# Kernel tuning notes

Hardware: AMD Instinct MI355X
Metric: run time of the kernel (lower is better)

## Reference

```python
import jax, jax.numpy as jnp
import numpy as np
from jax import lax

WIN = 15      # sliding window size
BINS = 64     # luminance histogram bins
ALPHA = 0.9   # local vs global histogram mix
LAM1 = 0.5    # a-channel (material) removal weight
LAM2 = 0.5    # b-channel (material) removal weight
EPS = 1e-6


def _box_sum(x, win):
    return lax.reduce_window(x, 0.0, lax.add, (1, win, win, 1), (1, 1, 1, 1), 'SAME')


def setup_inputs() -> dict:
    key = jax.random.key(0)
    u = jax.random.uniform(key, (4, 3, 512, 512), dtype=jnp.float32)
    L = u[:, 0] * 100.0                 # L in [0,100]
    a = u[:, 1] * 255.0 - 128.0         # a in [-128,127]
    b = u[:, 2] * 255.0 - 128.0         # b in [-128,127]
    return {"batch_lab_raw": jnp.stack([L, a, b], axis=1)}


def reference(batch_lab_raw):
    # Normalize channels
    Ln = jnp.clip(batch_lab_raw[:, 0] / 100.0, 0.0, 1.0)      # (B,H,W)
    an = (batch_lab_raw[:, 1] + 128.0) / 255.0                # (B,H,W)
    bn = (batch_lab_raw[:, 2] + 128.0) / 255.0                # (B,H,W)

    # --- windowed luminance histogram anomaly ---
    idx = jnp.clip((Ln * BINS).astype(jnp.int32), 0, BINS - 1)            # (B,H,W)
    onehot = jax.nn.one_hot(idx, BINS, dtype=Ln.dtype)                    # (B,H,W,K)
    cnt = _box_sum(onehot, WIN)                                           # (B,H,W,K)
    n = _box_sum(jnp.ones(Ln.shape + (1,), Ln.dtype), WIN)                # (B,H,W,1) valid-pixel count
    # probability of own bin within local window
    p_loc = jnp.take_along_axis(cnt / n, idx[..., None], axis=-1)[..., 0]  # (B,H,W)
    # global per-image histogram probability of own bin
    p_glob_bins = jnp.mean(onehot, axis=(1, 2))                            # (B,K)
    p_glob = jnp.einsum('bhwk,bk->bhw', onehot, p_glob_bins)              # (B,H,W)

    S = -jnp.log(ALPHA * p_loc + (1.0 - ALPHA) * p_glob + EPS)            # surprise
    S_min = jnp.min(S, axis=(1, 2), keepdims=True)
    S_max = jnp.max(S, axis=(1, 2), keepdims=True)
    L_anom_norm = (S - S_min) / (S_max - S_min + EPS)                     # (B,H,W)

    # --- de-materialized illumination: remove local chroma (material) variation ---
    mu_a = _box_sum(an[..., None], WIN)[..., 0] / n[..., 0]
    mu_b = _box_sum(bn[..., None], WIN)[..., 0] / n[..., 0]
    L_perp = jnp.clip(Ln - LAM1 * (an - mu_a) - LAM2 * (bn - mu_b), 0.0, 1.0)

    return (L_perp[:, None], L_anom_norm[:, None])  # each (B,1,H,W)
```

## Files before the change

kernel.cpp:

```cpp
#include <hip/hip_runtime.h>

#define Hh 512
#define Ww 512
#define NPIX (Hh*Ww)
#define BATCH 4


__global__ __launch_bounds__(256) void k_hist(const float* __restrict__ in,
                                              unsigned* __restrict__ hp) {
    __shared__ unsigned lh[64];
    const int tid = threadIdx.x;
    if (tid < 64) lh[tid] = 0u;
    __syncthreads();
    const int img = blockIdx.x >> 6, sub = blockIdx.x & 63;
    const float4* Lp = (const float4*)(in + (size_t)img * 3 * NPIX) + sub * 1024;
    #pragma unroll
    for (int t = 0; t < 4; ++t) {
        float4 v = Lp[t*256 + tid];
        float f[4] = {v.x, v.y, v.z, v.w};
        #pragma unroll
        for (int j = 0; j < 4; ++j) {
            float ln = fminf(fmaxf(f[j] / 100.0f, 0.0f), 1.0f);
            int idx = min((int)(ln * 64.0f), 63);
            atomicAdd(&lh[idx], 1u);
        }
    }
    __syncthreads();
    if (tid < 64) hp[((size_t)img*64 + tid)*64 + sub] = lh[tid];
}

__global__ __launch_bounds__(256, 4) void k_main(const float* __restrict__ in,
        const unsigned* __restrict__ hp, float* __restrict__ bmin,
        float* __restrict__ bmax, float* __restrict__ out)
{
    __shared__ unsigned s_pk[78*9];
    __shared__ float s_c[78*36];
    __shared__ float s_cc[64*33];
    __shared__ float s_lnc[64*16];
    __shared__ float lhf[64];
    __shared__ float red[8];

    const int tx = threadIdx.x, ty = threadIdx.y;
    const int tid = ty*16 + tx;
    const int bx = blockIdx.x * 16, by = blockIdx.y * 64;
    const int img = blockIdx.z;
    const float* Lp = in + (size_t)img * 3 * NPIX;

    {
        const int bin = tid >> 2, grp = tid & 3;
        const uint4* p = (const uint4*)(hp + ((size_t)img*64 + bin)*64 + grp*16);
        uint4 x0 = p[0], x1 = p[1], x2 = p[2], x3 = p[3];
        unsigned sum = x0.x+x0.y+x0.z+x0.w + x1.x+x1.y+x1.z+x1.w
                     + x2.x+x2.y+x2.z+x2.w + x3.x+x3.y+x3.z+x3.w;
        sum += __shfl_xor(sum, 1);
        sum += __shfl_xor(sum, 2);
        if (grp == 0) lhf[bin] = (float)sum * (1.0f/262144.0f);
    }

    const int s = tx + 1;
    const int j0 = s >> 2;
    const unsigned m20 = 0x7FFFu << (s & 3);
    unsigned wm[5];
    #pragma unroll
    for (int i = 0; i < 5; ++i) {
        unsigned n = (m20 >> (4*i)) & 0xFu;
        wm[i] = (n&1u)*0x80u | (n&2u)*0x4000u | (n&4u)*0x200000u | (n&8u)*0x10000000u;
    }

    float4 Lv[3], Av[3], Bv[3];
    bool vld[3];
    #pragma unroll
    for (int it = 0; it < 3; ++it) {
        const int l = tid + it*256;
        const int r = l >> 3, c4 = l & 7;
        const int gy = by - 7 + r, gx0 = bx - 8 + c4*4;
        vld[it] = (l < 624) && gy >= 0 && gy < Hh && gx0 >= 0 && gx0 < Ww;
        if (vld[it]) {
            const int g = gy*Ww + gx0;
            Lv[it] = *(const float4*)(Lp + g);
            Av[it] = *(const float4*)(Lp + NPIX + g);
            Bv[it] = *(const float4*)(Lp + 2*NPIX + g);
        }
    }
    #pragma unroll
    for (int it = 0; it < 3; ++it) {
        const int l = tid + it*256;
        if (l < 624) {
            const int r = l >> 3, c4 = l & 7;
            unsigned pk = 0x7F7F7F7Fu;
            float4 cv = {0.f, 0.f, 0.f, 0.f};
            if (vld[it]) {
                const float l0 = fminf(fmaxf(Lv[it].x / 100.0f, 0.0f), 1.0f);
                const float l1 = fminf(fmaxf(Lv[it].y / 100.0f, 0.0f), 1.0f);
                const float l2 = fminf(fmaxf(Lv[it].z / 100.0f, 0.0f), 1.0f);
                const float l3 = fminf(fmaxf(Lv[it].w / 100.0f, 0.0f), 1.0f);
                const int b0 = min((int)(l0*64.0f), 63), b1 = min((int)(l1*64.0f), 63);
                const int b2 = min((int)(l2*64.0f), 63), b3 = min((int)(l3*64.0f), 63);
                pk = (unsigned)b0 | ((unsigned)b1<<8) | ((unsigned)b2<<16) | ((unsigned)b3<<24);
                const float k255 = 1.0f/255.0f;
                cv.x = (Av[it].x+128.0f)*k255 + (Bv[it].x+128.0f)*k255;
                cv.y = (Av[it].y+128.0f)*k255 + (Bv[it].y+128.0f)*k255;
                cv.z = (Av[it].z+128.0f)*k255 + (Bv[it].z+128.0f)*k255;
                cv.w = (Av[it].w+128.0f)*k255 + (Bv[it].w+128.0f)*k255;
                if (r >= 7 && r < 71 && c4 >= 2 && c4 <= 5) {
                    float4 lv4 = {l0, l1, l2, l3};
                    *(float4*)&s_lnc[(r-7)*16 + 4*(c4-2)] = lv4;
                }
            }
            s_pk[r*9 + c4] = pk;
            *(float4*)&s_c[r*36 + c4*4] = cv;
        }
    }
    __syncthreads();

    if (tid < 248) {
        const int grp = tid / 31;
        const int col = tid - grp*31;
        const int r0v = grp*8;
        float sum = 0.f;
        #pragma unroll
        for (int k = 0; k < 15; ++k) sum += s_c[(r0v+k)*36 + col];
        s_cc[r0v*33 + col] = sum;
        #pragma unroll
        for (int jj = 1; jj < 8; ++jj) {
            sum += s_c[(r0v+14+jj)*36 + col] - s_c[(r0v+jj-1)*36 + col];
            s_cc[(r0v+jj)*33 + col] = sum;
        }
    }
    __syncthreads();

    const int r0 = 4*ty;
    const int cb_dw = (tx+8) >> 2, cb_sh = 8*((tx+8)&3);
    unsigned cbb[4], cb4[4];
    #pragma unroll
    for (int j = 0; j < 4; ++j) {
        cbb[j] = (s_pk[(r0+7+j)*9 + cb_dw] >> cb_sh) & 0xFFu;
        cb4[j] = cbb[j] * 0x01010101u;
    }
    const unsigned K = 0x7F7F7F7Fu;
    int acc[4] = {0,0,0,0};
    const unsigned* rp = s_pk + r0*9 + j0;

    #pragma unroll
    for (int k = 0; k < 18; ++k) {
        const unsigned d0 = rp[k*9+0], d1 = rp[k*9+1], d2 = rp[k*9+2],
                       d3 = rp[k*9+3], d4 = rp[k*9+4];
        #pragma unroll
        for (int j = 0; j < 4; ++j) {
            if (j <= k && k <= j + 14) {
                acc[j] += __popc(~((d0^cb4[j])+K) & wm[0]);
                acc[j] += __popc(~((d1^cb4[j])+K) & wm[1]);
                acc[j] += __popc(~((d2^cb4[j])+K) & wm[2]);
                acc[j] += __popc(~((d3^cb4[j])+K) & wm[3]);
                acc[j] += __popc(~((d4^cb4[j])+K) & wm[4]);
            }
        }
    }

    float sc[4] = {0.f, 0.f, 0.f, 0.f};
    #pragma unroll
    for (int j = 0; j < 4; ++j) {
        const float* ccp = s_cc + (r0+j)*33 + s;
        #pragma unroll
        for (int dx = 0; dx < 15; ++dx) sc[j] += ccp[dx];
    }

    const int gx = bx + tx;
    const int cols = min(gx+7, Ww-1) - max(gx-7, 0) + 1;
    float* outN = out + (size_t)BATCH*NPIX;
    float smin = __builtin_inff(), smax = -__builtin_inff();
    #pragma unroll
    for (int j = 0; j < 4; ++j) {
        const int gy = by + r0 + j;
        const int rows = min(gy+7, Hh-1) - max(gy-7, 0) + 1;
        const float invn = __builtin_amdgcn_rcpf((float)(rows*cols));
        const float S = -__logf(0.9f*((float)acc[j]*invn) + 0.1f*lhf[cbb[j]] + 1e-6f);
        const int gbase = img*NPIX + gy*Ww + gx;
        outN[gbase] = S;
        const float lp = s_lnc[(r0+j)*16 + tx]
                       - 0.5f*(s_c[(r0+7+j)*36 + tx+8] - sc[j]*invn);
        out[gbase] = fminf(fmaxf(lp, 0.f), 1.f);
        smin = fminf(smin, S); smax = fmaxf(smax, S);
    }

    #pragma unroll
    for (int off = 32; off >= 1; off >>= 1) {
        smin = fminf(smin, __shfl_xor(smin, off));
        smax = fmaxf(smax, __shfl_xor(smax, off));
    }
    const int wid = tid >> 6;
    if ((tid & 63) == 0) { red[wid] = smin; red[4+wid] = smax; }
    __syncthreads();
    if (tid == 0) {
        const int bid = blockIdx.y*32 + blockIdx.x;
        bmin[img*256 + bid] = fminf(fminf(red[0],red[1]), fminf(red[2],red[3]));
        bmax[img*256 + bid] = fmaxf(fmaxf(red[4],red[5]), fmaxf(red[6],red[7]));
    }
}

__global__ __launch_bounds__(256) void k_norm(float* __restrict__ outN,
        const float* __restrict__ bmin, const float* __restrict__ bmax) {
    __shared__ float red[2];
    const int tid = threadIdx.x;
    const int img = blockIdx.x >> 8;

    if (tid < 64) {
        float4 a = ((const float4*)(bmin + img*256))[tid];
        float4 b = ((const float4*)(bmax + img*256))[tid];
        float mn = fminf(fminf(a.x, a.y), fminf(a.z, a.w));
        float mx = fmaxf(fmaxf(b.x, b.y), fmaxf(b.z, b.w));
        #pragma unroll
        for (int off = 32; off >= 1; off >>= 1) {
            mn = fminf(mn, __shfl_xor(mn, off));
            mx = fmaxf(mx, __shfl_xor(mx, off));
        }
        if (tid == 0) { red[0] = mn; red[1] = mx; }
    }
    __syncthreads();
    const float vmin = red[0];
    const float inv = 1.0f / (red[1] - vmin + 1e-6f);

    float4* p = (float4*)outN + (size_t)blockIdx.x*256;
    float4 v = p[tid];
    v.x = (v.x - vmin) * inv; v.y = (v.y - vmin) * inv;
    v.z = (v.z - vmin) * inv; v.w = (v.w - vmin) * inv;
    p[tid] = v;
}

extern "C" void kernel_launch(void* const* d_in, const int* in_sizes, int n_in,
                              void* d_out, int out_size, void* d_ws, size_t ws_size,
                              hipStream_t stream) {
    const float* in = (const float*)d_in[0];
    float* out = (float*)d_out;
    float* bmin = (float*)d_ws;
    float* bmax = bmin + BATCH*256;
    unsigned* hp = (unsigned*)(bmax + BATCH*256);

    k_hist<<<BATCH*64, 256, 0, stream>>>(in, hp);
    dim3 grid(Ww/16, Hh/64, BATCH), blk(16, 16);
    k_main<<<grid, blk, 0, stream>>>(in, hp, bmin, bmax, out);
    k_norm<<<BATCH*256, 256, 0, stream>>>(out + (size_t)BATCH*NPIX, bmin, bmax);
}
```

Baseline: 86.69 us.

## Retile main kernel to square 32x32 tiles with 2x2 outputs per thread

Result: faster. 84.70 us (-2.3%).

```diff
diff --git a/kernel.cpp b/kernel.cpp
--- a/kernel.cpp
+++ b/kernel.cpp
@@ -33,16 +33,16 @@
         const unsigned* __restrict__ hp, float* __restrict__ bmin,
         float* __restrict__ bmax, float* __restrict__ out)
 {
-    __shared__ unsigned s_pk[78*9];
-    __shared__ float s_c[78*36];
-    __shared__ float s_cc[64*33];
-    __shared__ float s_lnc[64*16];
+    __shared__ unsigned s_pk[46*13];
+    __shared__ float s_c[46*50];
+    __shared__ float s_cc[32*49];
+    __shared__ float s_lnc[32*32];
     __shared__ float lhf[64];
     __shared__ float red[8];
 
     const int tx = threadIdx.x, ty = threadIdx.y;
     const int tid = ty*16 + tx;
-    const int bx = blockIdx.x * 16, by = blockIdx.y * 64;
+    const int bx = blockIdx.x * 32, by = blockIdx.y * 32;
     const int img = blockIdx.z;
     const float* Lp = in + (size_t)img * 3 * NPIX;
 
@@ -72,9 +72,9 @@
     #pragma unroll
     for (int it = 0; it < 3; ++it) {
         const int l = tid + it*256;
-        const int r = l >> 3, c4 = l & 7;
+        const int r = l / 12, c4 = l - r*12;
         const int gy = by - 7 + r, gx0 = bx - 8 + c4*4;
-        vld[it] = (l < 624) && gy >= 0 && gy < Hh && gx0 >= 0 && gx0 < Ww;
+        vld[it] = (l < 552) && gy >= 0 && gy < Hh && gx0 >= 0 && gx0 < Ww;
         if (vld[it]) {
             const int g = gy*Ww + gx0;
             Lv[it] = *(const float4*)(Lp + g);
@@ -85,8 +85,8 @@
     #pragma unroll
     for (int it = 0; it < 3; ++it) {
         const int l = tid + it*256;
-        if (l < 624) {
-            const int r = l >> 3, c4 = l & 7;
+        if (l < 552) {
+            const int r = l / 12, c4 = l - r*12;
             unsigned pk = 0x7F7F7F7Fu;
             float4 cv = {0.f, 0.f, 0.f, 0.f};
             if (vld[it]) {
@@ -102,87 +102,115 @@
                 cv.y = (Av[it].y+128.0f)*k255 + (Bv[it].y+128.0f)*k255;
                 cv.z = (Av[it].z+128.0f)*k255 + (Bv[it].z+128.0f)*k255;
                 cv.w = (Av[it].w+128.0f)*k255 + (Bv[it].w+128.0f)*k255;
-                if (r >= 7 && r < 71 && c4 >= 2 && c4 <= 5) {
+                if (r >= 7 && r < 39 && c4 >= 2 && c4 <= 9) {
                     float4 lv4 = {l0, l1, l2, l3};
-                    *(float4*)&s_lnc[(r-7)*16 + 4*(c4-2)] = lv4;
+                    *(float4*)&s_lnc[(r-7)*32 + 4*(c4-2)] = lv4;
                 }
             }
-            s_pk[r*9 + c4] = pk;
-            *(float4*)&s_c[r*36 + c4*4] = cv;
-        }
-    }
-    __syncthreads();
-
-    if (tid < 248) {
-        const int grp = tid / 31;
-        const int col = tid - grp*31;
-        const int r0v = grp*8;
-        float sum = 0.f;
+            s_pk[r*13 + c4] = pk;
+            *(float4*)&s_c[r*50 + c4*4] = cv;
+        }
+    }
+    __syncthreads();
+
+    #pragma unroll
+    for (int l0i = 0; l0i < 3; ++l0i) {
+        const int l = tid + l0i*256;
+        const int q = l & 15, c = l >> 4;
+        float mid = 0.f;
         #pragma unroll
-        for (int k = 0; k < 15; ++k) sum += s_c[(r0v+k)*36 + col];
-        s_cc[r0v*33 + col] = sum;
-        #pragma unroll
-        for (int jj = 1; jj < 8; ++jj) {
-            sum += s_c[(r0v+14+jj)*36 + col] - s_c[(r0v+jj-1)*36 + col];
-            s_cc[(r0v+jj)*33 + col] = sum;
-        }
-    }
-    __syncthreads();
-
-    const int r0 = 4*ty;
-    const int cb_dw = (tx+8) >> 2, cb_sh = 8*((tx+8)&3);
-    unsigned cbb[4], cb4[4];
-    #pragma unroll
-    for (int j = 0; j < 4; ++j) {
-        cbb[j] = (s_pk[(r0+7+j)*9 + cb_dw] >> cb_sh) & 0xFFu;
-        cb4[j] = cbb[j] * 0x01010101u;
-    }
+        for (int k = 1; k < 15; ++k) mid += s_c[(2*q+k)*50 + c];
+        s_cc[(2*q)*49 + c]   = mid + s_c[(2*q)*50 + c];
+        s_cc[(2*q+1)*49 + c] = mid + s_c[(2*q+15)*50 + c];
+    }
+    __syncthreads();
+
+    const int r0 = 2*ty;
+    const int dwA = (tx+8) >> 2,  shA = 8*((tx+8)&3);
+    const int dwB = (tx+24) >> 2, shB = 8*((tx+24)&3);
+    const unsigned binA0 = (s_pk[(r0+7)*13 + dwA] >> shA) & 0xFFu;
+    const unsigned binA1 = (s_pk[(r0+8)*13 + dwA] >> shA) & 0xFFu;
+    const unsigned binB0 = (s_pk[(r0+7)*13 + dwB] >> shB) & 0xFFu;
+    const unsigned binB1 = (s_pk[(r0+8)*13 + dwB] >> shB) & 0xFFu;
+    const unsigned cA0 = binA0*0x01010101u, cA1 = binA1*0x01010101u;
+    const unsigned cB0 = binB0*0x01010101u, cB1 = binB1*0x01010101u;
     const unsigned K = 0x7F7F7F7Fu;
-    int acc[4] = {0,0,0,0};
-    const unsigned* rp = s_pk + r0*9 + j0;
-
-    #pragma unroll
-    for (int k = 0; k < 18; ++k) {
-        const unsigned d0 = rp[k*9+0], d1 = rp[k*9+1], d2 = rp[k*9+2],
-                       d3 = rp[k*9+3], d4 = rp[k*9+4];
-        #pragma unroll
-        for (int j = 0; j < 4; ++j) {
-            if (j <= k && k <= j + 14) {
-                acc[j] += __popc(~((d0^cb4[j])+K) & wm[0]);
-                acc[j] += __popc(~((d1^cb4[j])+K) & wm[1]);
-                acc[j] += __popc(~((d2^cb4[j])+K) & wm[2]);
-                acc[j] += __popc(~((d3^cb4[j])+K) & wm[3]);
-                acc[j] += __popc(~((d4^cb4[j])+K) & wm[4]);
-            }
-        }
-    }
-
-    float sc[4] = {0.f, 0.f, 0.f, 0.f};
-    #pragma unroll
-    for (int j = 0; j < 4; ++j) {
-        const float* ccp = s_cc + (r0+j)*33 + s;
-        #pragma unroll
-        for (int dx = 0; dx < 15; ++dx) sc[j] += ccp[dx];
-    }
-
-    const int gx = bx + tx;
-    const int cols = min(gx+7, Ww-1) - max(gx-7, 0) + 1;
+    int pA0=0, qA0=0, pA1=0, qA1=0, pB0=0, qB0=0, pB1=0, qB1=0;
+    const unsigned* rp = s_pk + r0*13 + j0;
+
+    #pragma unroll
+    for (int k = 0; k < 16; ++k) {
+        const unsigned d0 = rp[k*13+0], d1 = rp[k*13+1], d2 = rp[k*13+2],
+                       d3 = rp[k*13+3], d4 = rp[k*13+4], d5 = rp[k*13+5],
+                       d6 = rp[k*13+6], d7 = rp[k*13+7], d8 = rp[k*13+8];
+        if (k != 15) {
+            pA0 += __popc(~((d0^cA0)+K) & wm[0]);
+            qA0 += __popc(~((d1^cA0)+K) & wm[1]);
+            pA0 += __popc(~((d2^cA0)+K) & wm[2]);
+            qA0 += __popc(~((d3^cA0)+K) & wm[3]);
+            pA0 += __popc(~((d4^cA0)+K) & wm[4]);
+            pB0 += __popc(~((d4^cB0)+K) & wm[0]);
+            qB0 += __popc(~((d5^cB0)+K) & wm[1]);
+            pB0 += __popc(~((d6^cB0)+K) & wm[2]);
+            qB0 += __popc(~((d7^cB0)+K) & wm[3]);
+            pB0 += __popc(~((d8^cB0)+K) & wm[4]);
+        }
+        if (k != 0) {
+            pA1 += __popc(~((d0^cA1)+K) & wm[0]);
+            qA1 += __popc(~((d1^cA1)+K) & wm[1]);
+            pA1 += __popc(~((d2^cA1)+K) & wm[2]);
+            qA1 += __popc(~((d3^cA1)+K) & wm[3]);
+            pA1 += __popc(~((d4^cA1)+K) & wm[4]);
+            pB1 += __popc(~((d4^cB1)+K) & wm[0]);
+            qB1 += __popc(~((d5^cB1)+K) & wm[1]);
+            pB1 += __popc(~((d6^cB1)+K) & wm[2]);
+            qB1 += __popc(~((d7^cB1)+K) & wm[3]);
+            pB1 += __popc(~((d8^cB1)+K) & wm[4]);
+        }
+    }
+    const int cntA0 = pA0+qA0, cntA1 = pA1+qA1, cntB0 = pB0+qB0, cntB1 = pB1+qB1;
+
+    float scA0 = 0.f, scA1 = 0.f, scB0 = 0.f, scB1 = 0.f;
+    const float* cc0 = s_cc + r0*49 + s;
+    const float* cc1 = cc0 + 49;
+    #pragma unroll
+    for (int dx = 0; dx < 15; ++dx) {
+        scA0 += cc0[dx];    scA1 += cc1[dx];
+        scB0 += cc0[16+dx]; scB1 += cc1[16+dx];
+    }
+
+    const int gxA = bx + tx, gxB = gxA + 16;
+    const int gy0 = by + r0;
+    const int colsA = min(gxA+7, Ww-1) - max(gxA-7, 0) + 1;
+    const int colsB = min(gxB+7, Ww-1) - max(gxB-7, 0) + 1;
+    const int rows0 = min(gy0+7, Hh-1) - max(gy0-7, 0) + 1;
+    const int rows1 = min(gy0+8, Hh-1) - max(gy0-6, 0) + 1;
+    const float iA0 = __builtin_amdgcn_rcpf((float)(rows0*colsA));
+    const float iA1 = __builtin_amdgcn_rcpf((float)(rows1*colsA));
+    const float iB0 = __builtin_amdgcn_rcpf((float)(rows0*colsB));
+    const float iB1 = __builtin_amdgcn_rcpf((float)(rows1*colsB));
+    const float SA0 = -__logf(0.9f*((float)cntA0*iA0) + 0.1f*lhf[binA0] + 1e-6f);
+    const float SA1 = -__logf(0.9f*((float)cntA1*iA1) + 0.1f*lhf[binA1] + 1e-6f);
+    const float SB0 = -__logf(0.9f*((float)cntB0*iB0) + 0.1f*lhf[binB0] + 1e-6f);
+    const float SB1 = -__logf(0.9f*((float)cntB1*iB1) + 0.1f*lhf[binB1] + 1e-6f);
+    const int gbase = img*NPIX + gy0*Ww + gxA;
     float* outN = out + (size_t)BATCH*NPIX;
-    float smin = __builtin_inff(), smax = -__builtin_inff();
-    #pragma unroll
-    for (int j = 0; j < 4; ++j) {
-        const int gy = by + r0 + j;
-        const int rows = min(gy+7, Hh-1) - max(gy-7, 0) + 1;
-        const float invn = __builtin_amdgcn_rcpf((float)(rows*cols));
-        const float S = -__logf(0.9f*((float)acc[j]*invn) + 0.1f*lhf[cbb[j]] + 1e-6f);
-        const int gbase = img*NPIX + gy*Ww + gx;
-        outN[gbase] = S;
-        const float lp = s_lnc[(r0+j)*16 + tx]
-                       - 0.5f*(s_c[(r0+7+j)*36 + tx+8] - sc[j]*invn);
-        out[gbase] = fminf(fmaxf(lp, 0.f), 1.f);
-        smin = fminf(smin, S); smax = fmaxf(smax, S);
-    }
-
+    outN[gbase]          = SA0;
+    outN[gbase + 16]     = SB0;
+    outN[gbase + Ww]     = SA1;
+    outN[gbase + Ww + 16]= SB1;
+
+    const float lpA0 = s_lnc[r0*32 + tx]       - 0.5f*(s_c[(r0+7)*50 + tx+8]  - scA0*iA0);
+    const float lpA1 = s_lnc[(r0+1)*32 + tx]   - 0.5f*(s_c[(r0+8)*50 + tx+8]  - scA1*iA1);
+    const float lpB0 = s_lnc[r0*32 + tx+16]    - 0.5f*(s_c[(r0+7)*50 + tx+24] - scB0*iB0);
+    const float lpB1 = s_lnc[(r0+1)*32 + tx+16]- 0.5f*(s_c[(r0+8)*50 + tx+24] - scB1*iB1);
+    out[gbase]           = fminf(fmaxf(lpA0, 0.f), 1.f);
+    out[gbase + 16]      = fminf(fmaxf(lpB0, 0.f), 1.f);
+    out[gbase + Ww]      = fminf(fmaxf(lpA1, 0.f), 1.f);
+    out[gbase + Ww + 16] = fminf(fmaxf(lpB1, 0.f), 1.f);
+
+    float smin = fminf(fminf(SA0, SA1), fminf(SB0, SB1));
+    float smax = fmaxf(fmaxf(SA0, SA1), fmaxf(SB0, SB1));
     #pragma unroll
     for (int off = 32; off >= 1; off >>= 1) {
         smin = fminf(smin, __shfl_xor(smin, off));
@@ -192,7 +220,7 @@
     if ((tid & 63) == 0) { red[wid] = smin; red[4+wid] = smax; }
     __syncthreads();
     if (tid == 0) {
-        const int bid = blockIdx.y*32 + blockIdx.x;
+        const int bid = blockIdx.y*16 + blockIdx.x;
         bmin[img*256 + bid] = fminf(fminf(red[0],red[1]), fminf(red[2],red[3]));
         bmax[img*256 + bid] = fmaxf(fmaxf(red[4],red[5]), fmaxf(red[6],red[7]));
     }
@@ -237,7 +265,7 @@
     unsigned* hp = (unsigned*)(bmax + BATCH*256);
 
     k_hist<<<BATCH*64, 256, 0, stream>>>(in, hp);
-    dim3 grid(Ww/16, Hh/64, BATCH), blk(16, 16);
+    dim3 grid(Ww/32, Hh/32, BATCH), blk(16, 16);
     k_main<<<grid, blk, 0, stream>>>(in, hp, bmin, bmax, out);
     k_norm<<<BATCH*256, 256, 0, stream>>>(out + (size_t)BATCH*NPIX, bmin, bmax);
 }
```
